# Kernel optimization log

Measured on AMD Instinct MI355X. Metric: run time of the kernel, lower is better.

## Reference

```python
import jax, jax.numpy as jnp
import numpy as np

N = 50000        # nodes
E = 800000       # edges
F_IN = 32        # float features (x also carries 1 trailing cell-id column)
CELL_DIM = 16
NUM_CELLS = 854
C = 64           # out_channels
H0, H1 = 2, 1    # heads schedule for num_layers=2 -> [2, 1]
D_IN = F_IN + CELL_DIM  # 48, GAT input dim after cell embedding concat
NEG_SLOPE = 0.2  # PyG GATConv default negative_slope


def setup_inputs() -> dict:
    key = jax.random.key(0)
    ks = jax.random.split(key, 14)
    base = jax.random.normal(ks[0], (N, F_IN), jnp.float32)
    cell_ids = jax.random.randint(ks[1], (N,), 0, NUM_CELLS)
    x = jnp.concatenate([base, cell_ids.astype(jnp.float32)[:, None]], axis=1)
    edge_index = jax.random.randint(ks[2], (2, E), 0, N, dtype=jnp.int32)
    s = lambda f: 1.0 / np.sqrt(f)
    emb = jax.random.normal(ks[3], (NUM_CELLS, CELL_DIM), jnp.float32)
    W0 = jax.random.normal(ks[4], (D_IN, H0 * C), jnp.float32) * s(D_IN)
    a_src0 = jax.random.normal(ks[5], (H0, C), jnp.float32) * s(C)
    a_dst0 = jax.random.normal(ks[6], (H0, C), jnp.float32) * s(C)
    b0 = jnp.zeros((C,), jnp.float32)
    ln_g = jnp.ones((C,), jnp.float32)
    ln_b = jnp.zeros((C,), jnp.float32)
    W1 = jax.random.normal(ks[7], (C, H1 * C), jnp.float32) * s(C)
    a_src1 = jax.random.normal(ks[8], (H1, C), jnp.float32) * s(C)
    a_dst1 = jax.random.normal(ks[9], (H1, C), jnp.float32) * s(C)
    b1 = jnp.zeros((C,), jnp.float32)
    return {"x": x, "edge_index": edge_index, "emb": emb,
            "W0": W0, "a_src0": a_src0, "a_dst0": a_dst0, "b0": b0,
            "ln_g": ln_g, "ln_b": ln_b,
            "W1": W1, "a_src1": a_src1, "a_dst1": a_dst1, "b1": b1}


def gat_layer(h_in, src, dst, W, a_src, a_dst, b, heads):
    # h_in: [N, D]; src/dst: [E'] (self-loops already appended)
    h = (h_in @ W).reshape(N, heads, C)                 # [N, H, C]
    alpha_s = jnp.einsum('nhc,hc->nh', h, a_src)        # [N, H]
    alpha_d = jnp.einsum('nhc,hc->nh', h, a_dst)
    e = jax.nn.leaky_relu(alpha_s[src] + alpha_d[dst], NEG_SLOPE)  # [E', H]
    # segment softmax over incoming edges of each dst node
    m = jax.ops.segment_max(e, dst, num_segments=N)     # [N, H]
    ex = jnp.exp(e - m[dst])
    denom = jax.ops.segment_sum(ex, dst, num_segments=N)
    alpha = ex / denom[dst]                             # [E', H]
    msg = h[src] * alpha[:, :, None]                    # [E', H, C]
    out = jax.ops.segment_sum(msg, dst, num_segments=N) # [N, H, C]
    return out.mean(axis=1) + b                         # concat=False -> mean over heads


def layer_norm(x, g, b):
    mu = x.mean(-1, keepdims=True)
    var = ((x - mu) ** 2).mean(-1, keepdims=True)
    return (x - mu) * jax.lax.rsqrt(var + 1e-5) * g + b


def reference(x, edge_index, emb, W0, a_src0, a_dst0, b0, ln_g, ln_b,
              W1, a_src1, a_dst1, b1):
    base = x[:, :-1]
    cell_ids = x[:, -1].astype(jnp.int32)
    h = jnp.concatenate([base, emb[cell_ids]], axis=1)  # [N, 48]
    # add self-loops (PyG GATConv default add_self_loops=True)
    loop = jnp.arange(N, dtype=edge_index.dtype)
    src = jnp.concatenate([edge_index[0], loop])
    dst = jnp.concatenate([edge_index[1], loop])
    h = gat_layer(h, src, dst, W0, a_src0, a_dst0, b0, H0)
    h = jax.nn.elu(layer_norm(h, ln_g, ln_b))           # dropout is identity at eval
    h = gat_layer(h, src, dst, W1, a_src1, a_dst1, b1, H1)
    return h
```

## Files before the change

### kernel.cpp

```cpp
#include <hip/hip_runtime.h>
#include <hip/hip_bf16.h>

#define N_NODES 50000
#define N_EDGES 800000
#define E_TOT 850000
#define F_IN 32
#define CELL_DIM 16
#define D_IN 48
#define X_STRIDE 33
#define NUM_CELLS 854
#define NEG_SLOPE 0.2f
#define SCAN_BLOCKS 49
#define NODE0_BLOCKS 2048
#define MERGE_BLOCKS 1563
#define EDGE_BLOCKS 3125
#define NXCD 8
#define BWX 16
#define W 24
#define NP 12

typedef unsigned int uint;
typedef unsigned short ushort;

static __device__ __forceinline__ uint f2b(float f) {
  uint x = __float_as_uint(f);
  return (x + 0x7fffu + ((x >> 16) & 1u)) >> 16;
}
static __device__ __forceinline__ float b2f_lo(uint w) { return __uint_as_float(w << 16); }
static __device__ __forceinline__ float b2f_hi(uint w) { return __uint_as_float(w & 0xffff0000u); }
static __device__ __forceinline__ float lrelu(float e) { return fmaxf(e, NEG_SLOPE * e); }


__global__ __launch_bounds__(256) void k_bfill(const int* __restrict__ ei,
                                               int* __restrict__ cnt,
                                               ushort* __restrict__ bkt) {
  int e = blockIdx.x * 256 + threadIdx.x;
  if (e >= N_EDGES) return;
  uint xcc;
  asm volatile("s_getreg_b32 %0, hwreg(HW_REG_XCC_ID)" : "=s"(xcc));
  xcc &= (NXCD - 1);
  int s = ei[e], d = ei[N_EDGES + e];
  int p = atomicAdd(&cnt[xcc * N_NODES + d], 1);
  if (p < BWX) bkt[(xcc * N_NODES + d) * BWX + p] = (ushort)s;
}


__global__ __launch_bounds__(1024) void k_scan1(const int* __restrict__ cnt,
                                                int* __restrict__ off,
                                                int* __restrict__ bsum) {
  __shared__ int ws[16];
  int tid = threadIdx.x;
  int lane = tid & 63, wid = tid >> 6;
  int i = blockIdx.x * 1024 + tid;
  int v = 0;
  if (i < N_NODES) {
    v = 1;
#pragma unroll
    for (int x = 0; x < NXCD; ++x) v += min(cnt[x * N_NODES + i], BWX);
  }
  int sc = v;
#pragma unroll
  for (int o = 1; o < 64; o <<= 1) {
    int t = __shfl_up(sc, o, 64);
    if (lane >= o) sc += t;
  }
  if (lane == 63) ws[wid] = sc;
  __syncthreads();
  if (tid < 16) {
    int w = ws[tid];
    int s = w;
#pragma unroll
    for (int o = 1; o < 16; o <<= 1) {
      int t = __shfl_up(s, o, 64);
      if (tid >= o) s += t;
    }
    ws[tid] = s - w;
  }
  __syncthreads();
  int excl = sc - v + ws[wid];
  if (i < N_NODES) off[i] = excl;
  if (tid == 1023) bsum[blockIdx.x] = excl + v;
}

__global__ __launch_bounds__(1024) void k_scan23(int* __restrict__ off,
                                                 const int* __restrict__ bsum) {
  __shared__ int carry_s;
  int tid = threadIdx.x;
  if (tid < 64) {
    int v = (tid < SCAN_BLOCKS) ? bsum[tid] : 0;
    int s = v;
#pragma unroll
    for (int o = 1; o < 64; o <<= 1) {
      int t = __shfl_up(s, o, 64);
      if (tid >= o) s += t;
    }
    if (tid == (int)blockIdx.x) carry_s = s - v;
    if (blockIdx.x == 0 && tid == SCAN_BLOCKS - 1) off[N_NODES] = s;
  }
  __syncthreads();
  int carry = carry_s;
  int i = blockIdx.x * 1024 + tid;
  if (i < N_NODES) off[i] += carry;
}


__global__ __launch_bounds__(256) void k_node0(const float* __restrict__ x,
                                               const float* __restrict__ emb,
                                               const float* __restrict__ W0,
                                               const float* __restrict__ asrc,
                                               const float* __restrict__ adst,
                                               ushort* __restrict__ h0u,
                                               float* __restrict__ as0, float* __restrict__ ad0) {
  int tid = threadIdx.x;
  __shared__ float hin[8][48];
  int lane = tid & 63, wid = tid >> 6;
  int h = wid & 1;
  int q = wid >> 1;
  float w0r[D_IN];
#pragma unroll
  for (int k = 0; k < D_IN; ++k) w0r[k] = W0[k * 128 + h * 64 + lane];
  float av_s = asrc[h * 64 + lane], av_d = adst[h * 64 + lane];

  for (int g = blockIdx.x; g < N_NODES / 8; g += NODE0_BLOCKS) {
    int nb = g * 8;
#pragma unroll
    for (int j = 0; j < 2; ++j) {
      int loc = 2 * wid + j;
      int n = nb + loc;
      float t = 0.f;
      if (lane < 33) t = x[n * X_STRIDE + lane];
      int cid = (int)__shfl(t, 32, 64);
      cid = cid < 0 ? 0 : (cid >= NUM_CELLS ? NUM_CELLS - 1 : cid);
      if (lane >= 32 && lane < 48) t = emb[cid * CELL_DIM + (lane - 32)];
      if (lane < 48) hin[loc][lane] = t;
    }
    __syncthreads();
#pragma unroll
    for (int j = 0; j < 4; ++j) {
      int loc = 4 * q + j;
      int n = nb + loc;
      const float4* hp = (const float4*)hin[loc];
      float acc = 0.f;
#pragma unroll
      for (int k4 = 0; k4 < 12; ++k4) {
        float4 hh = hp[k4];
        acc = fmaf(hh.x, w0r[4 * k4 + 0], acc);
        acc = fmaf(hh.y, w0r[4 * k4 + 1], acc);
        acc = fmaf(hh.z, w0r[4 * k4 + 2], acc);
        acc = fmaf(hh.w, w0r[4 * k4 + 3], acc);
      }
      h0u[(n * 64 + lane) * 2 + h] = (ushort)f2b(acc);
      float sa = acc * av_s, sd = acc * av_d;
#pragma unroll
      for (int o = 32; o >= 1; o >>= 1) {
        sa += __shfl_xor(sa, o, 64);
        sd += __shfl_xor(sd, o, 64);
      }
      if (lane == 0) {
        as0[n * 2 + h] = sa;
        ad0[n * 2 + h] = sd;
      }
    }
    __syncthreads();
  }
}


__global__ __launch_bounds__(256) void k_merge(const int* __restrict__ cnt,
                                               const ushort* __restrict__ bkt,
                                               const int* __restrict__ off,
                                               const float2* __restrict__ as0v,
                                               const float2* __restrict__ ad0v,
                                               ushort* __restrict__ srcs,
                                               uint* __restrict__ wts) {
  int tid = threadIdx.x;
  int n = blockIdx.x * 32 + (tid >> 3);
  if (n >= N_NODES) return;
  int xg = tid & 7;
  int cx = min(cnt[xg * N_NODES + n], BWX);
  int sc = cx;
#pragma unroll
  for (int o = 1; o < 8; o <<= 1) {
    int t = __shfl_up(sc, o, 64);
    if ((tid & 7) >= o) sc += t;
  }
  int total = __shfl(sc, (tid & 63) | 7, 64);
  int base = off[n] + (sc - cx);
  float2 ad = ad0v[n];
  const ushort* src = bkt + (xg * N_NODES + n) * BWX;
  for (int k = 0; k < cx; ++k) {
    uint s = src[k];
    float2 a = as0v[s];
    uint wp = f2b(__expf(lrelu(a.x + ad.x))) | (f2b(__expf(lrelu(a.y + ad.y))) << 16);
    srcs[base + k] = (ushort)s;
    wts[base + k] = wp;
  }
  if (xg == 7) {
    float2 a = as0v[n];
    uint wp = f2b(__expf(lrelu(a.x + ad.x))) | (f2b(__expf(lrelu(a.y + ad.y))) << 16);
    int slot = off[n] + total;
    srcs[slot] = (ushort)n;
    wts[slot] = wp;
  }
}


__global__ __launch_bounds__(256) void k_agg0(const int* __restrict__ off,
                                              const ushort* __restrict__ srcs,
                                              const uint* __restrict__ wts,
                                              const uint* __restrict__ h0p,
                                              const float* __restrict__ b0,
                                              const float* __restrict__ lng,
                                              const float* __restrict__ lnb,
                                              const float* __restrict__ W1,
                                              const float* __restrict__ asrc1,
                                              const float* __restrict__ adst1,
                                              ushort* __restrict__ h1b,
                                              float* __restrict__ as1, float* __restrict__ ad1) {
  __shared__ uint gbuf[4][W * 64];
  __shared__ float yb[4][64];
  int tid = threadIdx.x;
  int lane = tid & 63, wl = tid >> 6;
  int n = blockIdx.x * 4 + wl;
  int i0 = off[n], i1 = off[n + 1];
  float acc0 = 0.f, acc1 = 0.f, den0 = 0.f, den1 = 0.f;
  uint* gb = gbuf[wl];

  for (int w0 = i0; w0 < i1; w0 += W) {
    int idx = w0 + lane;
    uint s = 0u, wy = 0u;
    if (lane < W && idx < i1) {
      s = (uint)srcs[idx];
      wy = wts[idx];
    }
#pragma unroll
    for (int j = 0; j < W; ++j) {
      uint sx = (uint)__builtin_amdgcn_readlane((int)s, j);
      __builtin_amdgcn_global_load_lds((const uint*)(h0p + sx * 64u + (uint)lane),
                                       gb + j * 64, 4, 0, 0);
    }
    asm volatile("s_waitcnt vmcnt(0)" ::: "memory");
    __builtin_amdgcn_sched_barrier(0);
#pragma unroll
    for (int j = 0; j < W; ++j) {
      uint wyj = (uint)__builtin_amdgcn_readlane((int)wy, j);
      uint h = gb[j * 64 + lane];
      float w;
      w = b2f_lo(wyj); acc0 += w * b2f_lo(h); den0 += w;
      w = b2f_hi(wyj); acc1 += w * b2f_hi(h); den1 += w;
    }
    asm volatile("s_waitcnt lgkmcnt(0)" ::: "memory");
    __builtin_amdgcn_sched_barrier(0);
  }

  float v = 0.5f * (acc0 / den0 + acc1 / den1) + b0[lane];
  float mu = v;
#pragma unroll
  for (int o = 32; o >= 1; o >>= 1) mu += __shfl_xor(mu, o, 64);
  mu *= (1.0f / 64.0f);
  float d = v - mu;
  float vr = d * d;
#pragma unroll
  for (int o = 32; o >= 1; o >>= 1) vr += __shfl_xor(vr, o, 64);
  vr *= (1.0f / 64.0f);
  float y = d * rsqrtf(vr + 1e-5f) * lng[lane] + lnb[lane];
  y = y > 0.f ? y : expm1f(y);
  yb[wl][lane] = y;
  const float4* yp = (const float4*)yb[wl];
  float q0 = 0.f, q1 = 0.f, q2 = 0.f, q3 = 0.f;
#pragma unroll
  for (int k4 = 0; k4 < 16; ++k4) {
    float4 yy = yp[k4];
    q0 = fmaf(yy.x, W1[(4 * k4 + 0) * 64 + lane], q0);
    q1 = fmaf(yy.y, W1[(4 * k4 + 1) * 64 + lane], q1);
    q2 = fmaf(yy.z, W1[(4 * k4 + 2) * 64 + lane], q2);
    q3 = fmaf(yy.w, W1[(4 * k4 + 3) * 64 + lane], q3);
  }
  float h1v = (q0 + q1) + (q2 + q3);
  h1b[n * 64 + lane] = (ushort)f2b(h1v);
  float sa = h1v * asrc1[lane];
  float sdv = h1v * adst1[lane];
#pragma unroll
  for (int o = 32; o >= 1; o >>= 1) {
    sa += __shfl_xor(sa, o, 64);
    sdv += __shfl_xor(sdv, o, 64);
  }
  if (lane == 0) {
    as1[n] = sa;
    ad1[n] = sdv;
  }
}


__global__ __launch_bounds__(256) void k_agg1(const int* __restrict__ off,
                                              const ushort* __restrict__ srcs,
                                              const ushort* __restrict__ h1b,
                                              const float* __restrict__ as1,
                                              const float* __restrict__ ad1,
                                              const float* __restrict__ b1,
                                              float* __restrict__ out) {
  __shared__ uint gbuf[4][NP * 64];
  int tid = threadIdx.x;
  int lane = tid & 63, wl = tid >> 6;
  int n = blockIdx.x * 4 + wl;
  int i0 = off[n], i1 = off[n + 1];
  float adv = ad1[n];
  float acc = 0.f, den = 0.f;
  uint* gb = gbuf[wl];
  const ushort* gbs = (const ushort*)gb;
  uint hl = lane & 31;
  int half = lane >> 5;

  for (int w0 = i0; w0 < i1; w0 += W) {
    int idx = w0 + lane;
    uint s = 0u;
    float wv = 0.f;
    if (lane < W && idx < i1) {
      s = (uint)srcs[idx];
      wv = __expf(lrelu(as1[s] + adv));
    }
#pragma unroll
    for (int j = 0; j < NP; ++j) {
      uint sxA = (uint)__builtin_amdgcn_readlane((int)s, 2 * j);
      uint sxB = (uint)__builtin_amdgcn_readlane((int)s, 2 * j + 1);
      uint sx2 = half ? sxB : sxA;
      __builtin_amdgcn_global_load_lds((const uint*)(h1b + sx2 * 64u) + hl,
                                       gb + j * 64, 4, 0, 0);
    }
    asm volatile("s_waitcnt vmcnt(0)" ::: "memory");
    __builtin_amdgcn_sched_barrier(0);
#pragma unroll
    for (int j = 0; j < NP; ++j) {
      float wA = __uint_as_float(
          (uint)__builtin_amdgcn_readlane((int)__float_as_uint(wv), 2 * j));
      float wB = __uint_as_float(
          (uint)__builtin_amdgcn_readlane((int)__float_as_uint(wv), 2 * j + 1));
      uint hA = (uint)gbs[j * 128 + lane];
      uint hB = (uint)gbs[j * 128 + 64 + lane];
      acc = fmaf(wA, __uint_as_float(hA << 16), acc);
      den += wA;
      acc = fmaf(wB, __uint_as_float(hB << 16), acc);
      den += wB;
    }
    asm volatile("s_waitcnt lgkmcnt(0)" ::: "memory");
    __builtin_amdgcn_sched_barrier(0);
  }
  out[n * 64 + lane] = acc / den + b1[lane];
}


extern "C" void kernel_launch(void* const* d_in, const int* in_sizes, int n_in,
                              void* d_out, int out_size, void* d_ws, size_t ws_size,
                              hipStream_t stream) {
  const float* x    = (const float*)d_in[0];
  const int*   ei   = (const int*)d_in[1];
  const float* emb  = (const float*)d_in[2];
  const float* W0   = (const float*)d_in[3];
  const float* as0w = (const float*)d_in[4];
  const float* ad0w = (const float*)d_in[5];
  const float* b0   = (const float*)d_in[6];
  const float* lng  = (const float*)d_in[7];
  const float* lnb  = (const float*)d_in[8];
  const float* W1   = (const float*)d_in[9];
  const float* as1w = (const float*)d_in[10];
  const float* ad1w = (const float*)d_in[11];
  const float* b1   = (const float*)d_in[12];
  float* out = (float*)d_out;

  ushort* bkt  = (ushort*)d_ws;
  ushort* h1b  = (ushort*)d_ws;
  int*    cnt  = (int*)((char*)d_ws + (size_t)NXCD * N_NODES * BWX * 2);
  float*  as1  = (float*)cnt;
  float*  ad1  = as1 + N_NODES;
  int*    off  = (int*)((char*)cnt + (size_t)NXCD * N_NODES * 4);
  int*    bsum = off + N_NODES + 1;
  ushort* srcs = (ushort*)(bsum + 64);
  uint*   wts  = (uint*)(srcs + E_TOT);
  float*  as0  = (float*)(wts + E_TOT);
  float*  ad0  = as0 + N_NODES * 2;
  uint*   h0p  = (uint*)(ad0 + N_NODES * 2);

  hipMemsetAsync(cnt, 0, NXCD * N_NODES * sizeof(int), stream);
  k_bfill<<<EDGE_BLOCKS, 256, 0, stream>>>(ei, cnt, bkt);
  k_scan1<<<SCAN_BLOCKS, 1024, 0, stream>>>(cnt, off, bsum);
  k_scan23<<<SCAN_BLOCKS, 1024, 0, stream>>>(off, bsum);
  k_node0<<<NODE0_BLOCKS, 256, 0, stream>>>(x, emb, W0, as0w, ad0w, (ushort*)h0p, as0, ad0);
  k_merge<<<MERGE_BLOCKS, 256, 0, stream>>>(cnt, bkt, off, (const float2*)as0,
                                            (const float2*)ad0, srcs, wts);
  k_agg0<<<N_NODES / 4, 256, 0, stream>>>(off, srcs, wts, h0p, b0, lng, lnb, W1,
                                          as1w, ad1w, h1b, as1, ad1);
  k_agg1<<<N_NODES / 4, 256, 0, stream>>>(off, srcs, h1b, as1, ad1, b1, out);
}
```

Baseline: 250.0 us.

## Fuse bucket fill into node projection and replace scan with atomic allocation

Merges the edge-bucketing kernel into the layer-0 node projection kernel as extra blocks in a single launch. The two-pass prefix scan over node degrees is dropped. Instead, each merge block computes a local prefix and reserves space with one global atomicAdd, writing per-node (start, count) metadata that the aggregation kernels read. This removes three kernel launches and their serialization gaps. The cost is that CSR segments are no longer in node order, which may hurt locality, and the node projection now runs on half as many blocks.

Measured after the change: 240.0 us. -4.0%, faster.

```diff
diff --git a/kernel.cpp b/kernel.cpp
--- a/kernel.cpp
+++ b/kernel.cpp
@@ -10,8 +10,7 @@
 #define X_STRIDE 33
 #define NUM_CELLS 854
 #define NEG_SLOPE 0.2f
-#define SCAN_BLOCKS 49
-#define NODE0_BLOCKS 2048
+#define NODE0_BLOCKS 1024
 #define MERGE_BLOCKS 1563
 #define EDGE_BLOCKS 3125
 #define NXCD 8
@@ -31,87 +30,28 @@
 static __device__ __forceinline__ float lrelu(float e) { return fmaxf(e, NEG_SLOPE * e); }
 
 
-__global__ __launch_bounds__(256) void k_bfill(const int* __restrict__ ei,
-                                               int* __restrict__ cnt,
-                                               ushort* __restrict__ bkt) {
-  int e = blockIdx.x * 256 + threadIdx.x;
-  if (e >= N_EDGES) return;
-  uint xcc;
-  asm volatile("s_getreg_b32 %0, hwreg(HW_REG_XCC_ID)" : "=s"(xcc));
-  xcc &= (NXCD - 1);
-  int s = ei[e], d = ei[N_EDGES + e];
-  int p = atomicAdd(&cnt[xcc * N_NODES + d], 1);
-  if (p < BWX) bkt[(xcc * N_NODES + d) * BWX + p] = (ushort)s;
-}
-
-
-__global__ __launch_bounds__(1024) void k_scan1(const int* __restrict__ cnt,
-                                                int* __restrict__ off,
-                                                int* __restrict__ bsum) {
-  __shared__ int ws[16];
+__global__ __launch_bounds__(256) void k_nb(const float* __restrict__ x,
+                                            const float* __restrict__ emb,
+                                            const float* __restrict__ W0,
+                                            const float* __restrict__ asrc,
+                                            const float* __restrict__ adst,
+                                            const int* __restrict__ ei,
+                                            ushort* __restrict__ h0u,
+                                            float* __restrict__ as0, float* __restrict__ ad0,
+                                            int* __restrict__ cnt, ushort* __restrict__ bkt) {
   int tid = threadIdx.x;
-  int lane = tid & 63, wid = tid >> 6;
-  int i = blockIdx.x * 1024 + tid;
-  int v = 0;
-  if (i < N_NODES) {
-    v = 1;
-#pragma unroll
-    for (int x = 0; x < NXCD; ++x) v += min(cnt[x * N_NODES + i], BWX);
-  }
-  int sc = v;
-#pragma unroll
-  for (int o = 1; o < 64; o <<= 1) {
-    int t = __shfl_up(sc, o, 64);
-    if (lane >= o) sc += t;
-  }
-  if (lane == 63) ws[wid] = sc;
-  __syncthreads();
-  if (tid < 16) {
-    int w = ws[tid];
-    int s = w;
-#pragma unroll
-    for (int o = 1; o < 16; o <<= 1) {
-      int t = __shfl_up(s, o, 64);
-      if (tid >= o) s += t;
-    }
-    ws[tid] = s - w;
-  }
-  __syncthreads();
-  int excl = sc - v + ws[wid];
-  if (i < N_NODES) off[i] = excl;
-  if (tid == 1023) bsum[blockIdx.x] = excl + v;
-}
-
-__global__ __launch_bounds__(1024) void k_scan23(int* __restrict__ off,
-                                                 const int* __restrict__ bsum) {
-  __shared__ int carry_s;
-  int tid = threadIdx.x;
-  if (tid < 64) {
-    int v = (tid < SCAN_BLOCKS) ? bsum[tid] : 0;
-    int s = v;
-#pragma unroll
-    for (int o = 1; o < 64; o <<= 1) {
-      int t = __shfl_up(s, o, 64);
-      if (tid >= o) s += t;
-    }
-    if (tid == (int)blockIdx.x) carry_s = s - v;
-    if (blockIdx.x == 0 && tid == SCAN_BLOCKS - 1) off[N_NODES] = s;
-  }
-  __syncthreads();
-  int carry = carry_s;
-  int i = blockIdx.x * 1024 + tid;
-  if (i < N_NODES) off[i] += carry;
-}
-
-
-__global__ __launch_bounds__(256) void k_node0(const float* __restrict__ x,
-                                               const float* __restrict__ emb,
-                                               const float* __restrict__ W0,
-                                               const float* __restrict__ asrc,
-                                               const float* __restrict__ adst,
-                                               ushort* __restrict__ h0u,
-                                               float* __restrict__ as0, float* __restrict__ ad0) {
-  int tid = threadIdx.x;
+  if (blockIdx.x >= NODE0_BLOCKS) {
+    int e = (blockIdx.x - NODE0_BLOCKS) * 256 + tid;
+    if (e < N_EDGES) {
+      uint xcc;
+      asm volatile("s_getreg_b32 %0, hwreg(HW_REG_XCC_ID)" : "=s"(xcc));
+      xcc &= (NXCD - 1);
+      int s = ei[e], d = ei[N_EDGES + e];
+      int p = atomicAdd(&cnt[xcc * N_NODES + d], 1);
+      if (p < BWX) bkt[(xcc * N_NODES + d) * BWX + p] = (ushort)s;
+    }
+    return;
+  }
   __shared__ float hin[8][48];
   int lane = tid & 63, wid = tid >> 6;
   int h = wid & 1;
@@ -168,16 +108,20 @@
 
 __global__ __launch_bounds__(256) void k_merge(const int* __restrict__ cnt,
                                                const ushort* __restrict__ bkt,
-                                               const int* __restrict__ off,
                                                const float2* __restrict__ as0v,
                                                const float2* __restrict__ ad0v,
+                                               int* __restrict__ galloc,
+                                               int2* __restrict__ meta,
                                                ushort* __restrict__ srcs,
                                                uint* __restrict__ wts) {
+  __shared__ int gpre[32];
+  __shared__ int bbase;
   int tid = threadIdx.x;
-  int n = blockIdx.x * 32 + (tid >> 3);
-  if (n >= N_NODES) return;
+  int grp = tid >> 3;
+  int n = blockIdx.x * 32 + grp;
+  bool alive = (n < N_NODES);
   int xg = tid & 7;
-  int cx = min(cnt[xg * N_NODES + n], BWX);
+  int cx = alive ? min(cnt[xg * N_NODES + n], BWX) : 0;
   int sc = cx;
 #pragma unroll
   for (int o = 1; o < 8; o <<= 1) {
@@ -185,7 +129,24 @@
     if ((tid & 7) >= o) sc += t;
   }
   int total = __shfl(sc, (tid & 63) | 7, 64);
-  int base = off[n] + (sc - cx);
+  int items = alive ? total + 1 : 0;
+  if (xg == 7) gpre[grp] = items;
+  __syncthreads();
+  if (tid < 32) {
+    int v = gpre[tid];
+    int s = v;
+#pragma unroll
+    for (int o = 1; o < 32; o <<= 1) {
+      int t = __shfl_up(s, o, 64);
+      if (tid >= o) s += t;
+    }
+    gpre[tid] = s - v;
+    if (tid == 31) bbase = atomicAdd(galloc, s);
+  }
+  __syncthreads();
+  if (!alive) return;
+  int start = bbase + gpre[grp];
+  int base = start + (sc - cx);
   float2 ad = ad0v[n];
   const ushort* src = bkt + (xg * N_NODES + n) * BWX;
   for (int k = 0; k < cx; ++k) {
@@ -198,14 +159,14 @@
   if (xg == 7) {
     float2 a = as0v[n];
     uint wp = f2b(__expf(lrelu(a.x + ad.x))) | (f2b(__expf(lrelu(a.y + ad.y))) << 16);
-    int slot = off[n] + total;
-    srcs[slot] = (ushort)n;
-    wts[slot] = wp;
-  }
-}
-
-
-__global__ __launch_bounds__(256) void k_agg0(const int* __restrict__ off,
+    srcs[start + total] = (ushort)n;
+    wts[start + total] = wp;
+    meta[n] = make_int2(start, items);
+  }
+}
+
+
+__global__ __launch_bounds__(256) void k_agg0(const int2* __restrict__ meta,
                                               const ushort* __restrict__ srcs,
                                               const uint* __restrict__ wts,
                                               const uint* __restrict__ h0p,
@@ -222,7 +183,8 @@
   int tid = threadIdx.x;
   int lane = tid & 63, wl = tid >> 6;
   int n = blockIdx.x * 4 + wl;
-  int i0 = off[n], i1 = off[n + 1];
+  int2 mt = meta[n];
+  int i0 = mt.x, i1 = mt.x + mt.y;
   float acc0 = 0.f, acc1 = 0.f, den0 = 0.f, den1 = 0.f;
   uint* gb = gbuf[wl];
 
@@ -292,7 +254,7 @@
 }
 
 
-__global__ __launch_bounds__(256) void k_agg1(const int* __restrict__ off,
+__global__ __launch_bounds__(256) void k_agg1(const int2* __restrict__ meta,
                                               const ushort* __restrict__ srcs,
                                               const ushort* __restrict__ h1b,
                                               const float* __restrict__ as1,
@@ -303,7 +265,8 @@
   int tid = threadIdx.x;
   int lane = tid & 63, wl = tid >> 6;
   int n = blockIdx.x * 4 + wl;
-  int i0 = off[n], i1 = off[n + 1];
+  int2 mt = meta[n];
+  int i0 = mt.x, i1 = mt.x + mt.y;
   float adv = ad1[n];
   float acc = 0.f, den = 0.f;
   uint* gb = gbuf[wl];
@@ -367,27 +330,25 @@
   const float* b1   = (const float*)d_in[12];
   float* out = (float*)d_out;
 
-  ushort* bkt  = (ushort*)d_ws;
-  ushort* h1b  = (ushort*)d_ws;
-  int*    cnt  = (int*)((char*)d_ws + (size_t)NXCD * N_NODES * BWX * 2);
-  float*  as1  = (float*)cnt;
-  float*  ad1  = as1 + N_NODES;
-  int*    off  = (int*)((char*)cnt + (size_t)NXCD * N_NODES * 4);
-  int*    bsum = off + N_NODES + 1;
-  ushort* srcs = (ushort*)(bsum + 64);
-  uint*   wts  = (uint*)(srcs + E_TOT);
-  float*  as0  = (float*)(wts + E_TOT);
-  float*  ad0  = as0 + N_NODES * 2;
-  uint*   h0p  = (uint*)(ad0 + N_NODES * 2);
-
-  hipMemsetAsync(cnt, 0, NXCD * N_NODES * sizeof(int), stream);
-  k_bfill<<<EDGE_BLOCKS, 256, 0, stream>>>(ei, cnt, bkt);
-  k_scan1<<<SCAN_BLOCKS, 1024, 0, stream>>>(cnt, off, bsum);
-  k_scan23<<<SCAN_BLOCKS, 1024, 0, stream>>>(off, bsum);
-  k_node0<<<NODE0_BLOCKS, 256, 0, stream>>>(x, emb, W0, as0w, ad0w, (ushort*)h0p, as0, ad0);
-  k_merge<<<MERGE_BLOCKS, 256, 0, stream>>>(cnt, bkt, off, (const float2*)as0,
-                                            (const float2*)ad0, srcs, wts);
-  k_agg0<<<N_NODES / 4, 256, 0, stream>>>(off, srcs, wts, h0p, b0, lng, lnb, W1,
+  ushort* bkt    = (ushort*)d_ws;
+  ushort* h1b    = (ushort*)d_ws;
+  int*    cnt    = (int*)((char*)d_ws + (size_t)NXCD * N_NODES * BWX * 2);
+  int*    galloc = cnt + NXCD * N_NODES;
+  float*  as1    = (float*)cnt;
+  float*  ad1    = as1 + N_NODES;
+  int2*   meta   = (int2*)(galloc + 2);
+  ushort* srcs   = (ushort*)(meta + N_NODES);
+  uint*   wts    = (uint*)(srcs + E_TOT);
+  float*  as0    = (float*)(wts + E_TOT);
+  float*  ad0    = as0 + N_NODES * 2;
+  uint*   h0p    = (uint*)(ad0 + N_NODES * 2);
+
+  hipMemsetAsync(cnt, 0, (NXCD * N_NODES + 2) * sizeof(int), stream);
+  k_nb<<<NODE0_BLOCKS + EDGE_BLOCKS, 256, 0, stream>>>(x, emb, W0, as0w, ad0w, ei,
+                                                       (ushort*)h0p, as0, ad0, cnt, bkt);
+  k_merge<<<MERGE_BLOCKS, 256, 0, stream>>>(cnt, bkt, (const float2*)as0,
+                                            (const float2*)ad0, galloc, meta, srcs, wts);
+  k_agg0<<<N_NODES / 4, 256, 0, stream>>>(meta, srcs, wts, h0p, b0, lng, lnb, W1,
                                           as1w, ad1w, h1b, as1, ad1);
-  k_agg1<<<N_NODES / 4, 256, 0, stream>>>(off, srcs, h1b, as1, ad1, b1, out);
-}
+  k_agg1<<<N_NODES / 4, 256, 0, stream>>>(meta, srcs, h1b, as1, ad1, b1, out);
+}
```
